# Optimization experiments

Measured on AMD Instinct MI355X. Metric: run time of the kernel, lower is better.

The kernel has to match this reference:

```python
import jax, jax.numpy as jnp
import numpy as np

P = 7            # cfg.PATCH_SIZE_PHOTOMETRIC
BRIGHT = 0.02    # bright_threshold
BIG = 1e9        # masks invalid points out of kNN
K = 5            # neighbors for smoothness/slope


def _smooth_l1(x, y, beta):
    d = jnp.abs(x - y)
    return jnp.where(d < beta, 0.5 * d * d / beta, d - 0.5 * beta)


def _sample_patches(img, kp):
    # img: [B,1,H,W], kp: [B,N,2] (x,y) in pixel coords -> [B,1,N,P,P]
    # matches F.grid_sample(align_corners=True, bilinear, border): with the
    # module's normalization, sampling positions are exactly pixel coords.
    B, _, H, W = img.shape
    N = kp.shape[1]
    half = P // 2
    lin = jnp.linspace(-half, half, P)
    oy, ox = jnp.meshgrid(lin, lin, indexing='ij')  # patch index (i,j): +x=lin[j], +y=lin[i]
    px = jnp.clip(kp[..., 0:1] + ox.ravel(), 0.0, W - 1)  # [B,N,P*P]
    py = jnp.clip(kp[..., 1:2] + oy.ravel(), 0.0, H - 1)
    x0 = jnp.floor(px); y0 = jnp.floor(py)
    fx = px - x0; fy = py - y0
    x0i = jnp.clip(x0.astype(jnp.int32), 0, W - 1)
    x1i = jnp.clip(x0i + 1, 0, W - 1)
    y0i = jnp.clip(y0.astype(jnp.int32), 0, H - 1)
    y1i = jnp.clip(y0i + 1, 0, H - 1)
    im = img[:, 0]  # [B,H,W]
    b = jnp.arange(B)[:, None, None]
    v00 = im[b, y0i, x0i]; v01 = im[b, y0i, x1i]
    v10 = im[b, y1i, x0i]; v11 = im[b, y1i, x1i]
    val = (v00 * (1 - fx) + v01 * fx) * (1 - fy) + (v10 * (1 - fx) + v11 * fx) * fy
    return val.reshape(B, 1, N, P, P)


def _forward(lg, rg, kpl, kpr, scores, Q):
    B, N, _ = kpl.shape
    # ---- epipolar ----
    y_diff = jnp.abs(kpl[..., 1] - kpr[..., 1])
    ws = scores.sum()
    l_epipolar = jnp.where(ws > 1e-4, (y_diff * scores).sum() / jnp.maximum(ws, 1e-12), y_diff.mean())
    # ---- photometric + intensity ----
    pl = _sample_patches(lg, kpl)
    pr = _sample_patches(rg, kpr)
    c = P // 2
    center_l = pl[:, 0, :, c, c]  # [B,N]
    center_r = pr[:, 0, :, c, c]
    is_bright = (center_l > BRIGHT).astype(pl.dtype)
    diff = jnp.abs(pl - pr).mean(axis=(1, 3, 4))  # [B,N]
    w = scores * is_bright
    wsum = w.sum()
    safe = jnp.maximum(wsum, 1e-12)
    l_masked = jnp.where(wsum > 1e-4, (diff * w).sum() / safe, 0.0)
    l_intensity = jnp.where(wsum > 1e-4, (_smooth_l1(center_l, center_r, 1.0) * w).sum() / safe, 0.0)
    l_photo = l_masked + l_intensity
    # ---- disparity -> 3D ----
    disp = kpl[..., 0] - kpr[..., 0]
    pts4 = jnp.concatenate([kpl, disp[..., None], jnp.ones((B, N, 1), kpl.dtype)], axis=-1)
    proj = jnp.einsum('bni,bji->bnj', pts4, Q)
    Wc = jnp.maximum(proj[..., 3], 1e-6)
    p3d = proj[..., :3] / Wc[..., None]  # [B,N,3]
    Z = p3d[..., 2]
    valid = (Z > 100) & (Z < 30000) & (scores > 0.1)  # [B,N]
    # ---- kNN smoothness / slope / zero-mean (masked, vectorized) ----
    pm = p3d / 1000.0
    xy = pm[..., jnp.array([0, 2])]  # [B,N,2] horizontal plane
    h = pm[..., 1]                   # [B,N] height
    sq = (xy * xy).sum(-1)
    d2 = sq[:, :, None] + sq[:, None, :] - 2.0 * jnp.einsum('bnd,bmd->bnm', xy, xy)
    dist = jnp.sqrt(jnp.maximum(d2, 1e-12))  # [B,N,N]
    vm = valid[:, :, None] & valid[:, None, :]
    dist = jnp.where(vm, dist, BIG)
    negd, idx = jax.lax.top_k(-dist, K + 1)   # ascending distance
    nbr_idx = idx[:, :, 1:]                   # drop self
    nbr_d = jnp.maximum(-negd[:, :, 1:], 1e-3)
    b = jnp.arange(B)[:, None, None]
    nbr_h = h[b, nbr_idx]                     # [B,N,K]
    local_mean = nbr_h.mean(-1)
    n_valid = valid.sum(-1)
    nv = jnp.maximum(n_valid, 1).astype(h.dtype)
    vf = valid.astype(h.dtype)
    ls_b = (_smooth_l1(h, local_mean, 0.01) * vf).sum(-1) / nv
    slopes = jnp.abs(nbr_h - h[..., None]) / nbr_d
    pen = jax.nn.relu(slopes - 0.4)
    lsl_b = (pen * vf[..., None]).sum((-1, -2)) / (nv * K)
    lz_b = jnp.abs((h * vf).sum(-1) / nv)
    ok = (n_valid >= 10).astype(h.dtype)
    nb = jnp.maximum(ok.sum(), 1.0)
    gate = ((scores > 0.1).sum() >= 10) & (ok.sum() > 0)
    l_smooth = jnp.where(gate, (ls_b * ok).sum() / nb, 0.0)
    l_slope = jnp.where(gate, (lsl_b * ok).sum() / nb, 0.0)
    l_zeromean = jnp.where(gate, (lz_b * ok).sum() / nb, 0.0)
    return (l_photo, l_epipolar, l_smooth, l_slope, l_zeromean)


def setup_inputs() -> dict:
    key = jax.random.key(0)
    k = jax.random.split(key, 7)
    B, N, H, W = 16, 2000, 720, 1280
    lg = jax.random.uniform(k[0], (B, 1, H, W), dtype=jnp.float32)
    rg = jax.random.uniform(k[1], (B, 1, H, W), dtype=jnp.float32)
    kx = jax.random.uniform(k[2], (B, N), minval=200.0, maxval=1080.0)
    ky = jax.random.uniform(k[3], (B, N), minval=50.0, maxval=670.0)
    disp = jax.random.uniform(k[4], (B, N), minval=10.0, maxval=200.0)
    kpl = jnp.stack([kx, ky], -1)
    kpr = jnp.stack([kx - disp, ky + 0.5 * jax.random.normal(k[5], (B, N))], -1)
    scores = jax.random.uniform(k[6], (B, N), dtype=jnp.float32)
    f, cx, cy, Tx = 1000.0, 640.0, 360.0, 120.0  # focal px, principal point, baseline mm
    Qm = jnp.array([[1.0, 0.0, 0.0, -cx],
                    [0.0, 1.0, 0.0, -cy],
                    [0.0, 0.0, 0.0, f],
                    [0.0, 0.0, 1.0 / Tx, 0.0]], dtype=jnp.float32)
    Q = jnp.broadcast_to(Qm, (B, 4, 4))
    return {"lg": lg, "rg": rg, "kpl": kpl, "kpr": kpr, "scores": scores, "Q": Q}


def reference(lg, rg, kpl, kpr, scores, Q):
    return _forward(lg, rg, kpl, kpr, scores, Q)
```

## Files before the change

kernel.cpp:

```cpp
#include <hip/hip_runtime.h>

#define BB 16
#define NN 2000
#define HH 720
#define WW 1280
#define NPT (BB*NN)
#define PB_BLOCKS (NPT/4)
#define PROJ_BLOCKS (NPT/256)
#define KSTRIDE 2048
#define MAX_SEG 500

static __device__ __forceinline__ unsigned u_min(unsigned a, unsigned b){ return a < b ? a : b; }

static __device__ __forceinline__ unsigned u_med3(unsigned a, unsigned b, unsigned c) {
    unsigned d;
    asm("v_med3_u32 %0, %1, %2, %3" : "=v"(d) : "v"(a), "v"(b), "v"(c));
    return d;
}

__device__ __forceinline__ void ins5(unsigned K[5], unsigned u) {
    K[4] = u_med3(K[3], K[4], u);
    K[3] = u_med3(K[2], K[3], u);
    K[2] = u_med3(K[1], K[2], u);
    K[1] = u_med3(K[0], K[1], u);
    K[0] = u_min(K[0], u);
}

__device__ __forceinline__ float bilin(const float* __restrict__ im, float px, float py) {
    px = fminf(fmaxf(px, 0.f), (float)(WW - 1));
    py = fminf(fmaxf(py, 0.f), (float)(HH - 1));
    float x0f = floorf(px), y0f = floorf(py);
    float fx = px - x0f, fy = py - y0f;
    int x0 = min(max((int)x0f, 0), WW - 1);
    int x1 = min(x0 + 1, WW - 1);
    int y0 = min(max((int)y0f, 0), HH - 1);
    int y1 = min(y0 + 1, HH - 1);
    const float* r0 = im + (size_t)y0 * WW;
    const float* r1 = im + (size_t)y1 * WW;
    float v00 = r0[x0], v01 = r0[x1], v10 = r1[x0], v11 = r1[x1];
    return (v00 * (1.f - fx) + v01 * fx) * (1.f - fy)
         + (v10 * (1.f - fx) + v11 * fx) * fy;
}

__global__ __launch_bounds__(256) void project_kernel(
    const float* __restrict__ kpl, const float* __restrict__ kpr,
    const float* __restrict__ scores, const float* __restrict__ Q,
    float4* __restrict__ pts, float* __restrict__ partialsA,
    float* __restrict__ batch_acc, unsigned* __restrict__ dcnt)
{
    if (blockIdx.x == 0) {
        if (threadIdx.x < BB * 4) batch_acc[threadIdx.x] = 0.f;
        if (threadIdx.x == BB * 4) *dcnt = 0u;
    }
    int pt = blockIdx.x * 256 + threadIdx.x;
    int b  = pt / NN;

    float2 kl = ((const float2* __restrict__)kpl)[pt];
    float2 kr = ((const float2* __restrict__)kpr)[pt];
    float sc  = scores[pt];
    float ydiff = fabsf(kl.y - kr.y);

    const float* q = Q + b * 16;
    float dsp = kl.x - kr.x;
    float p0 = q[0]*kl.x  + q[1]*kl.y  + q[2]*dsp  + q[3];
    float p1 = q[4]*kl.x  + q[5]*kl.y  + q[6]*dsp  + q[7];
    float p2 = q[8]*kl.x  + q[9]*kl.y  + q[10]*dsp + q[11];
    float p3 = q[12]*kl.x + q[13]*kl.y + q[14]*dsp + q[15];
    float Wc = fmaxf(p3, 1e-6f);
    float X = p0 / Wc, Y = p1 / Wc, Z = p2 / Wc;
    bool valid = (Z > 100.f) && (Z < 30000.f) && (sc > 0.1f);
    float x  = X / 1000.f;
    float hh = Y / 1000.f;
    float y  = Z / 1000.f;
    float sq = x * x + y * y;
    if (!valid) { x = 0.f; y = 0.f; sq = 1e18f; }
    pts[pt] = make_float4(x, y, sq, hh);

    float s0 = sc, s1 = ydiff * sc, s2 = ydiff, s3 = (sc > 0.1f) ? 1.f : 0.f;
    #pragma unroll
    for (int off = 32; off > 0; off >>= 1) {
        s0 += __shfl_down(s0, off, 64);
        s1 += __shfl_down(s1, off, 64);
        s2 += __shfl_down(s2, off, 64);
        s3 += __shfl_down(s3, off, 64);
    }
    __shared__ float red[4][4];
    int wave = threadIdx.x >> 6, lane = threadIdx.x & 63;
    if (lane == 0) { red[wave][0]=s0; red[wave][1]=s1; red[wave][2]=s2; red[wave][3]=s3; }
    __syncthreads();
    if (threadIdx.x < 4) {
        int k = threadIdx.x;
        partialsA[blockIdx.x * 4 + k] = red[0][k] + red[1][k] + red[2][k] + red[3][k];
    }
}

__global__ __launch_bounds__(256) void fused_patch_scan(
    const float* __restrict__ lg, const float* __restrict__ rg,
    const float* __restrict__ kpl, const float* __restrict__ kpr,
    const float* __restrict__ scores,
    const float4* __restrict__ pts, unsigned* __restrict__ keybuf,
    float* __restrict__ partialsB, int msegLen, int lns, int interleave)
{
    int i = blockIdx.x;
    int pid, sid;
    if (interleave) {
        if ((i % 5) == 0) { sid = i / 5; pid = -1; }
        else { pid = (i / 5) * 4 + (i % 5) - 1; sid = -1; }
    } else {
        if (i < PB_BLOCKS) { pid = i; sid = -1; }
        else { pid = -1; sid = i - PB_BLOCKS; }
    }

    if (pid >= 0) {
        if (pid >= PB_BLOCKS) return;
        int wave = threadIdx.x >> 6, lane = threadIdx.x & 63;
        int rr = lane / 7, ci = lane - rr * 7;
        int s00 = lane + rr;
        if (s00 > 54) s00 = 54;
        int reg_r = lane >> 3, reg_c = lane & 7;

        int pt = pid * 4 + wave;
        int b = pt / NN;
        const float* iml = lg + (size_t)b * (HH * WW);
        const float* imr = rg + (size_t)b * (HH * WW);
        float kxl = kpl[2*pt], kyl = kpl[2*pt+1];
        float kxr = kpr[2*pt], kyr = kpr[2*pt+1];
        float sc  = scores[pt];

        float flx = floorf(kxl), fly = floorf(kyl);
        float frx = floorf(kxr), fry = floorf(kyr);
        int xbl = (int)flx - 3, ybl = (int)fly - 3;
        int xbr = (int)frx - 3, ybr = (int)fry - 3;
        float fxl = kxl - flx, fyl = kyl - fly;
        float fxr = kxr - frx, fyr = kyr - fry;
        bool inL = (xbl >= 0) && (xbl <= WW-8) && (ybl >= 0) && (ybl <= HH-8);
        bool inR = (xbr >= 0) && (xbr <= WW-8) && (ybr >= 0) && (ybr <= HH-8);

        float regL = 0.f, regR = 0.f;
        if (inL) regL = iml[(size_t)(ybl + reg_r) * WW + xbl + reg_c];
        if (inR) regR = imr[(size_t)(ybr + reg_r) * WW + xbr + reg_c];

        float vl = 0.f, vr = 0.f;
        if (inL) {
            float v00 = __shfl(regL, s00,     64);
            float v01 = __shfl(regL, s00 + 1, 64);
            float v10 = __shfl(regL, s00 + 8, 64);
            float v11 = __shfl(regL, s00 + 9, 64);
            vl = (v00*(1.f-fxl) + v01*fxl)*(1.f-fyl) + (v10*(1.f-fxl) + v11*fxl)*fyl;
        } else if (lane < 49) {
            vl = bilin(iml, kxl + (float)(ci-3), kyl + (float)(rr-3));
        }
        if (inR) {
            float v00 = __shfl(regR, s00,     64);
            float v01 = __shfl(regR, s00 + 1, 64);
            float v10 = __shfl(regR, s00 + 8, 64);
            float v11 = __shfl(regR, s00 + 9, 64);
            vr = (v00*(1.f-fxr) + v01*fxr)*(1.f-fyr) + (v10*(1.f-fxr) + v11*fxr)*fyr;
        } else if (lane < 49) {
            vr = bilin(imr, kxr + (float)(ci-3), kyr + (float)(rr-3));
        }

        float adiff = (lane < 49) ? fabsf(vl - vr) : 0.f;
        float cl = __shfl(vl, 24, 64);
        float cr = __shfl(vr, 24, 64);
        #pragma unroll
        for (int off = 32; off > 0; off >>= 1) adiff += __shfl_down(adiff, off, 64);

        __shared__ float red[4][3];
        if (lane == 0) {
            float isb = (cl > 0.02f) ? 1.f : 0.f;
            float w   = sc * isb;
            float dc  = fabsf(cl - cr);
            float sl1 = (dc < 1.f) ? 0.5f * dc * dc : dc - 0.5f;
            red[wave][0] = w;
            red[wave][1] = w * adiff * (1.f/49.f);
            red[wave][2] = sl1 * w;
        }
        __syncthreads();
        if (threadIdx.x < 4) {
            int k = threadIdx.x;
            float v = 0.f;
            if (k < 3) v = red[0][k] + red[1][k] + red[2][k] + red[3][k];
            partialsB[pid * 4 + k] = v;
        }
    } else {
        __shared__ float4 seg[MAX_SEG];
        int sblk = sid;
        int bx   = sblk & 7;
        int r    = sblk >> 3;
        int segi = r & ((1 << lns) - 1);
        int b    = r >> lns;
        int ns   = 1 << lns;
        int mseg0 = segi * msegLen;
        int n = bx * 256 + threadIdx.x;
        int nc = (n < NN) ? n : (NN - 1);

        const float4* cand = pts + b * NN + mseg0;
        for (int j = threadIdx.x; j < msegLen; j += 256) seg[j] = cand[j];

        float4 me = pts[b * NN + nc];
        float nx2 = -2.f * me.x, ny2 = -2.f * me.y, sqn = me.z;

        unsigned K[5] = {0xFFFFFFFFu,0xFFFFFFFFu,0xFFFFFFFFu,0xFFFFFFFFu,0xFFFFFFFFu};

        int nb0 = bx * 256;
        bool has_self = (mseg0 < nb0 + 256) && (mseg0 + msegLen > nb0);

        __syncthreads();

        if (has_self) {
            #pragma unroll 5
            for (int mm = 0; mm < msegLen; ++mm) {
                float4 o = seg[mm];
                int m = mseg0 + mm;
                float t = fmaf(ny2, o.y, o.z);
                t = fmaf(nx2, o.x, t);
                float d2 = fmaxf(t + sqn, 1e-12f);
                unsigned u = (__float_as_uint(d2) & 0xFFFFF800u) | (unsigned)m;
                u = (m == n) ? 0xFFFFFFFFu : u;
                ins5(K, u);
            }
        } else {
            #pragma unroll 5
            for (int mm = 0; mm < msegLen; ++mm) {
                float4 o = seg[mm];
                int m = mseg0 + mm;
                float t = fmaf(ny2, o.y, o.z);
                t = fmaf(nx2, o.x, t);
                float d2 = fmaxf(t + sqn, 1e-12f);
                unsigned u = (__float_as_uint(d2) & 0xFFFFF800u) | (unsigned)m;
                ins5(K, u);
            }
        }

        if (n < NN) {
            size_t base = (size_t)((b * ns + segi) * 5) * KSTRIDE + n;
            keybuf[base              ] = K[0];
            keybuf[base + KSTRIDE    ] = K[1];
            keybuf[base + KSTRIDE * 2] = K[2];
            keybuf[base + KSTRIDE * 3] = K[3];
            keybuf[base + KSTRIDE * 4] = K[4];
        }
    }
}

__global__ __launch_bounds__(256) void knn_merge_final(
    const float4* __restrict__ pts, const unsigned* __restrict__ keybuf,
    float* __restrict__ batch_acc, unsigned* __restrict__ dcnt,
    const float* __restrict__ partialsA, const float* __restrict__ partialsB,
    float* __restrict__ out, int ns)
{
    int b = blockIdx.y;
    int n = blockIdx.x * 256 + threadIdx.x;

    float ls = 0.f, pen = 0.f, hacc = 0.f, cnt = 0.f;
    if (n < NN) {
        float4 me = pts[b * NN + n];
        if (me.z < 1e17f) {
            unsigned K[5] = {0xFFFFFFFFu,0xFFFFFFFFu,0xFFFFFFFFu,0xFFFFFFFFu,0xFFFFFFFFu};
            for (int s = 0; s < ns; ++s) {
                #pragma unroll
                for (int j = 0; j < 5; ++j) {
                    unsigned u = keybuf[(size_t)((b * ns + s) * 5 + j) * KSTRIDE + n];
                    ins5(K, u);
                }
            }
            float hsum = 0.f;
            #pragma unroll
            for (int t = 0; t < 5; ++t) {
                int idx = (int)(K[t] & 2047u);
                float4 o = pts[b * NN + idx];
                float dot = me.x * o.x + me.y * o.y;
                float d2 = (me.z + o.z) - 2.f * dot;
                float nd = fmaxf(sqrtf(fmaxf(d2, 1e-12f)), 0.001f);
                hsum += o.w;
                pen  += fmaxf(fabsf(o.w - me.w) / nd - 0.4f, 0.f);
            }
            float lm = hsum / 5.f;
            float dd = fabsf(me.w - lm);
            ls = (dd < 0.01f) ? 0.5f * dd * dd / 0.01f : dd - 0.005f;
            hacc = me.w;
            cnt  = 1.f;
        }
    }

    #pragma unroll
    for (int off = 32; off > 0; off >>= 1) {
        ls   += __shfl_down(ls,   off, 64);
        pen  += __shfl_down(pen,  off, 64);
        hacc += __shfl_down(hacc, off, 64);
        cnt  += __shfl_down(cnt,  off, 64);
    }
    __shared__ float r2[4][4];
    int wave = threadIdx.x >> 6, lane = threadIdx.x & 63;
    if (lane == 0) { r2[wave][0]=cnt; r2[wave][1]=ls; r2[wave][2]=pen; r2[wave][3]=hacc; }
    __syncthreads();
    if (threadIdx.x == 0) {
        float tc = r2[0][0]+r2[1][0]+r2[2][0]+r2[3][0];
        float tl = r2[0][1]+r2[1][1]+r2[2][1]+r2[3][1];
        float tp = r2[0][2]+r2[1][2]+r2[2][2]+r2[3][2];
        float th = r2[0][3]+r2[1][3]+r2[2][3]+r2[3][3];
        atomicAdd(&batch_acc[b * 4 + 0], tc);
        atomicAdd(&batch_acc[b * 4 + 1], tl);
        atomicAdd(&batch_acc[b * 4 + 2], tp);
        atomicAdd(&batch_acc[b * 4 + 3], th);
    }

    __shared__ int lastf;
    __threadfence();
    if (threadIdx.x == 0) {
        unsigned old = atomicAdd(dcnt, 1u);
        lastf = (old == (unsigned)(8 * BB - 1)) ? 1 : 0;
    }
    __syncthreads();
    if (!lastf) return;
    __threadfence();

    float s[7] = {0,0,0,0,0,0,0};
    for (int rI = threadIdx.x; rI < PROJ_BLOCKS; rI += 256) {
        s[0] += partialsA[rI * 4 + 0];
        s[1] += partialsA[rI * 4 + 1];
        s[2] += partialsA[rI * 4 + 2];
        s[3] += partialsA[rI * 4 + 3];
    }
    for (int rI = threadIdx.x; rI < PB_BLOCKS; rI += 256) {
        s[4] += partialsB[rI * 4 + 0];
        s[5] += partialsB[rI * 4 + 1];
        s[6] += partialsB[rI * 4 + 2];
    }
    #pragma unroll
    for (int off = 32; off > 0; off >>= 1) {
        #pragma unroll
        for (int k = 0; k < 7; ++k) s[k] += __shfl_down(s[k], off, 64);
    }
    __shared__ float ws2[4][7];
    if (lane == 0) {
        #pragma unroll
        for (int k = 0; k < 7; ++k) ws2[wave][k] = s[k];
    }
    __syncthreads();
    if (threadIdx.x == 0) {
        float t[7];
        #pragma unroll
        for (int k = 0; k < 7; ++k)
            t[k] = ws2[0][k] + ws2[1][k] + ws2[2][k] + ws2[3][k];
        float ssc = t[0], yds = t[1], yd = t[2], cnts = t[3];
        float wsum = t[4], dw = t[5], iw = t[6];

        float l_epi = (ssc > 1e-4f) ? yds / fmaxf(ssc, 1e-12f) : yd / (float)NPT;
        float safe = fmaxf(wsum, 1e-12f);
        float l_photo = (wsum > 1e-4f) ? (dw / safe + iw / safe) : 0.f;

        float als = 0.f, alsl = 0.f, alz = 0.f, okc = 0.f;
        for (int bb = 0; bb < BB; ++bb) {
            float nvf  = __hip_atomic_load(&batch_acc[bb*4+0], __ATOMIC_RELAXED, __HIP_MEMORY_SCOPE_AGENT);
            float lsb  = __hip_atomic_load(&batch_acc[bb*4+1], __ATOMIC_RELAXED, __HIP_MEMORY_SCOPE_AGENT);
            float penb = __hip_atomic_load(&batch_acc[bb*4+2], __ATOMIC_RELAXED, __HIP_MEMORY_SCOPE_AGENT);
            float hb   = __hip_atomic_load(&batch_acc[bb*4+3], __ATOMIC_RELAXED, __HIP_MEMORY_SCOPE_AGENT);
            float nv = fmaxf(nvf, 1.f);
            float ok = (nvf >= 10.f) ? 1.f : 0.f;
            als  += ok * (lsb / nv);
            alsl += ok * (penb / (nv * 5.f));
            alz  += ok * fabsf(hb / nv);
            okc  += ok;
        }
        float nb = fmaxf(okc, 1.f);
        bool gate = (cnts >= 10.f) && (okc > 0.f);
        out[0] = l_photo;
        out[1] = l_epi;
        out[2] = gate ? als / nb : 0.f;
        out[3] = gate ? alsl / nb : 0.f;
        out[4] = gate ? alz / nb : 0.f;
    }
}

extern "C" void kernel_launch(void* const* d_in, const int* in_sizes, int n_in,
                              void* d_out, int out_size, void* d_ws, size_t ws_size,
                              hipStream_t stream)
{
    const float* lg     = (const float*)d_in[0];
    const float* rg     = (const float*)d_in[1];
    const float* kpl    = (const float*)d_in[2];
    const float* kpr    = (const float*)d_in[3];
    const float* scores = (const float*)d_in[4];
    const float* Q      = (const float*)d_in[5];
    float* out = (float*)d_out;

    char* ws = (char*)d_ws;
    float4*   pts       = (float4*)ws;
    float*    partialsA = (float*)(ws + 512000);
    float*    partialsB = (float*)(ws + 514048);
    float*    batch_acc = (float*)(ws + 645120);
    unsigned* dcnt      = (unsigned*)(ws + 645376);
    unsigned* keybuf    = (unsigned*)(ws + 645632);

    int ns = 16;
    if (ws_size < 645632 + (size_t)BB * 16 * 5 * KSTRIDE * 4) ns = 8;
    if (ws_size < 645632 + (size_t)BB *  8 * 5 * KSTRIDE * 4) ns = 4;
    int lns = (ns == 16) ? 4 : ((ns == 8) ? 3 : 2);
    int msegLen = NN / ns;
    int interleave = (ns == 16) ? 1 : 0;

    int nblk = interleave ? 10240 : (PB_BLOCKS + 8 * ns * BB);

    project_kernel<<<PROJ_BLOCKS, 256, 0, stream>>>(kpl, kpr, scores, Q,
                                                    pts, partialsA, batch_acc, dcnt);
    fused_patch_scan<<<nblk, 256, 0, stream>>>(
        lg, rg, kpl, kpr, scores, pts, keybuf, partialsB, msegLen, lns, interleave);
    knn_merge_final<<<dim3(8, BB), 256, 0, stream>>>(pts, keybuf, batch_acc, dcnt,
                                                     partialsA, partialsB, out, ns);
}
```

Baseline: 188.4 us.

## Sort keypoints by row and co-schedule patch and kNN waves per block

Adds a per-batch counting sort of keypoints by y row so that neighbouring patch-sampling waves touch nearby image rows, aiming for better cache locality. The fused kernel now runs 320-thread blocks: four waves sample patches and one wave does a 64-query kNN segment scan, in place of separate block types. Per-point partials are written as float4, which removes the block-level shared reduction but leaves the final reduction to sum 32000 entries. It costs an extra kernel launch, and the final single-block reduction becomes larger.

Result: slower. 218.1 us (+15.8%).

```diff
diff --git a/kernel.cpp b/kernel.cpp
--- a/kernel.cpp
+++ b/kernel.cpp
@@ -5,7 +5,6 @@
 #define HH 720
 #define WW 1280
 #define NPT (BB*NN)
-#define PB_BLOCKS (NPT/4)
 #define PROJ_BLOCKS (NPT/256)
 #define KSTRIDE 2048
 #define MAX_SEG 500
@@ -94,33 +93,71 @@
     }
 }
 
-__global__ __launch_bounds__(256) void fused_patch_scan(
+__global__ __launch_bounds__(256) void sort_kernel(
+    const float* __restrict__ kpl, int* __restrict__ order)
+{
+    int b = blockIdx.x;
+    __shared__ int hist[720];
+    __shared__ int wsum[4];
+    for (int i = threadIdx.x; i < 720; i += 256) hist[i] = 0;
+    __syncthreads();
+    for (int p = threadIdx.x; p < NN; p += 256) {
+        float y = kpl[2 * (b * NN + p) + 1];
+        int bin = min(max((int)y, 0), 719);
+        atomicAdd(&hist[bin], 1);
+    }
+    __syncthreads();
+    int tid = threadIdx.x, lane = tid & 63, wv = tid >> 6;
+    int h0 = 0, h1 = 0, h2 = 0;
+    if (tid < 240) { h0 = hist[tid*3]; h1 = hist[tid*3+1]; h2 = hist[tid*3+2]; }
+    int lsum = h0 + h1 + h2;
+    int pre = lsum;
+    #pragma unroll
+    for (int off = 1; off < 64; off <<= 1) {
+        int t = __shfl_up(pre, off, 64);
+        if (lane >= off) pre += t;
+    }
+    if (lane == 63) wsum[wv] = pre;
+    __syncthreads();
+    int woff = 0;
+    for (int k = 0; k < wv; ++k) woff += wsum[k];
+    int excl = woff + pre - lsum;
+    if (tid < 240) {
+        hist[tid*3    ] = excl;
+        hist[tid*3 + 1] = excl + h0;
+        hist[tid*3 + 2] = excl + h0 + h1;
+    }
+    __syncthreads();
+    for (int p = threadIdx.x; p < NN; p += 256) {
+        float y = kpl[2 * (b * NN + p) + 1];
+        int bin = min(max((int)y, 0), 719);
+        int pos = atomicAdd(&hist[bin], 1);
+        order[b * NN + pos] = b * NN + p;
+    }
+}
+
+__global__ __launch_bounds__(320) void fused_patch_scan(
     const float* __restrict__ lg, const float* __restrict__ rg,
     const float* __restrict__ kpl, const float* __restrict__ kpr,
     const float* __restrict__ scores,
     const float4* __restrict__ pts, unsigned* __restrict__ keybuf,
-    float* __restrict__ partialsB, int msegLen, int lns, int interleave)
+    float4* __restrict__ partialsB, const int* __restrict__ order,
+    int msegLen, int lns)
 {
-    int i = blockIdx.x;
-    int pid, sid;
-    if (interleave) {
-        if ((i % 5) == 0) { sid = i / 5; pid = -1; }
-        else { pid = (i / 5) * 4 + (i % 5) - 1; sid = -1; }
-    } else {
-        if (i < PB_BLOCKS) { pid = i; sid = -1; }
-        else { pid = -1; sid = i - PB_BLOCKS; }
-    }
-
-    if (pid >= 0) {
-        if (pid >= PB_BLOCKS) return;
-        int wave = threadIdx.x >> 6, lane = threadIdx.x & 63;
+    __shared__ float4 seg[MAX_SEG];
+    int wave = threadIdx.x >> 6, lane = threadIdx.x & 63;
+
+    if (wave < 4) {
+        int idx = blockIdx.x * 4 + wave;
+        if (idx >= NPT) return;
+        int pt = order[idx];
+        int b  = idx / NN;
+
         int rr = lane / 7, ci = lane - rr * 7;
         int s00 = lane + rr;
         if (s00 > 54) s00 = 54;
         int reg_r = lane >> 3, reg_c = lane & 7;
 
-        int pt = pid * 4 + wave;
-        int b = pt / NN;
         const float* iml = lg + (size_t)b * (HH * WW);
         const float* imr = rg + (size_t)b * (HH * WW);
         float kxl = kpl[2*pt], kyl = kpl[2*pt+1];
@@ -166,47 +203,36 @@
         #pragma unroll
         for (int off = 32; off > 0; off >>= 1) adiff += __shfl_down(adiff, off, 64);
 
-        __shared__ float red[4][3];
         if (lane == 0) {
             float isb = (cl > 0.02f) ? 1.f : 0.f;
             float w   = sc * isb;
             float dc  = fabsf(cl - cr);
             float sl1 = (dc < 1.f) ? 0.5f * dc * dc : dc - 0.5f;
-            red[wave][0] = w;
-            red[wave][1] = w * adiff * (1.f/49.f);
-            red[wave][2] = sl1 * w;
-        }
-        __syncthreads();
-        if (threadIdx.x < 4) {
-            int k = threadIdx.x;
-            float v = 0.f;
-            if (k < 3) v = red[0][k] + red[1][k] + red[2][k] + red[3][k];
-            partialsB[pid * 4 + k] = v;
+            partialsB[pt] = make_float4(w, w * adiff * (1.f/49.f), sl1 * w, 0.f);
         }
     } else {
-        __shared__ float4 seg[MAX_SEG];
-        int sblk = sid;
-        int bx   = sblk & 7;
-        int r    = sblk >> 3;
-        int segi = r & ((1 << lns) - 1);
+        int ns  = 1 << lns;
+        int sid = blockIdx.x;
+        if (sid >= 32 * ns * BB) return;
+        int bx2  = sid & 31;
+        int r    = sid >> 5;
+        int segi = r & (ns - 1);
         int b    = r >> lns;
-        int ns   = 1 << lns;
         int mseg0 = segi * msegLen;
-        int n = bx * 256 + threadIdx.x;
+
+        const float4* cand = pts + b * NN + mseg0;
+        for (int j = lane; j < msegLen; j += 64) seg[j] = cand[j];
+        asm volatile("s_waitcnt lgkmcnt(0)" ::: "memory");
+
+        int n  = bx2 * 64 + lane;
         int nc = (n < NN) ? n : (NN - 1);
-
-        const float4* cand = pts + b * NN + mseg0;
-        for (int j = threadIdx.x; j < msegLen; j += 256) seg[j] = cand[j];
-
         float4 me = pts[b * NN + nc];
         float nx2 = -2.f * me.x, ny2 = -2.f * me.y, sqn = me.z;
 
         unsigned K[5] = {0xFFFFFFFFu,0xFFFFFFFFu,0xFFFFFFFFu,0xFFFFFFFFu,0xFFFFFFFFu};
 
-        int nb0 = bx * 256;
-        bool has_self = (mseg0 < nb0 + 256) && (mseg0 + msegLen > nb0);
-
-        __syncthreads();
+        int nb0 = bx2 * 64;
+        bool has_self = (mseg0 < nb0 + 64) && (mseg0 + msegLen > nb0);
 
         if (has_self) {
             #pragma unroll 5
@@ -247,7 +273,7 @@
 __global__ __launch_bounds__(256) void knn_merge_final(
     const float4* __restrict__ pts, const unsigned* __restrict__ keybuf,
     float* __restrict__ batch_acc, unsigned* __restrict__ dcnt,
-    const float* __restrict__ partialsA, const float* __restrict__ partialsB,
+    const float* __restrict__ partialsA, const float4* __restrict__ partialsB,
     float* __restrict__ out, int ns)
 {
     int b = blockIdx.y;
@@ -323,10 +349,11 @@
         s[2] += partialsA[rI * 4 + 2];
         s[3] += partialsA[rI * 4 + 3];
     }
-    for (int rI = threadIdx.x; rI < PB_BLOCKS; rI += 256) {
-        s[4] += partialsB[rI * 4 + 0];
-        s[5] += partialsB[rI * 4 + 1];
-        s[6] += partialsB[rI * 4 + 2];
+    for (int rI = threadIdx.x; rI < NPT; rI += 256) {
+        float4 v = partialsB[rI];
+        s[4] += v.x;
+        s[5] += v.y;
+        s[6] += v.z;
     }
     #pragma unroll
     for (int off = 32; off > 0; off >>= 1) {
@@ -389,24 +416,27 @@
     char* ws = (char*)d_ws;
     float4*   pts       = (float4*)ws;
     float*    partialsA = (float*)(ws + 512000);
-    float*    partialsB = (float*)(ws + 514048);
-    float*    batch_acc = (float*)(ws + 645120);
-    unsigned* dcnt      = (unsigned*)(ws + 645376);
-    unsigned* keybuf    = (unsigned*)(ws + 645632);
+    int*      order     = (int*)(ws + 514048);
+    float4*   partialsB = (float4*)(ws + 642048);
+    float*    batch_acc = (float*)(ws + 1154048);
+    unsigned* dcnt      = (unsigned*)(ws + 1154304);
+    unsigned* keybuf    = (unsigned*)(ws + 1154560);
 
     int ns = 16;
-    if (ws_size < 645632 + (size_t)BB * 16 * 5 * KSTRIDE * 4) ns = 8;
-    if (ws_size < 645632 + (size_t)BB *  8 * 5 * KSTRIDE * 4) ns = 4;
+    if (ws_size < 1154560 + (size_t)BB * 16 * 5 * KSTRIDE * 4) ns = 8;
+    if (ws_size < 1154560 + (size_t)BB *  8 * 5 * KSTRIDE * 4) ns = 4;
     int lns = (ns == 16) ? 4 : ((ns == 8) ? 3 : 2);
     int msegLen = NN / ns;
-    int interleave = (ns == 16) ? 1 : 0;
-
-    int nblk = interleave ? 10240 : (PB_BLOCKS + 8 * ns * BB);
+
+    int nsActive = 32 * ns * BB;
+    int nblk = (NPT + 3) / 4;
+    if (nsActive > nblk) nblk = nsActive;
 
     project_kernel<<<PROJ_BLOCKS, 256, 0, stream>>>(kpl, kpr, scores, Q,
                                                     pts, partialsA, batch_acc, dcnt);
-    fused_patch_scan<<<nblk, 256, 0, stream>>>(
-        lg, rg, kpl, kpr, scores, pts, keybuf, partialsB, msegLen, lns, interleave);
+    sort_kernel<<<BB, 256, 0, stream>>>(kpl, order);
+    fused_patch_scan<<<nblk, 320, 0, stream>>>(
+        lg, rg, kpl, kpr, scores, pts, keybuf, partialsB, order, msegLen, lns);
     knn_merge_final<<<dim3(8, BB), 256, 0, stream>>>(pts, keybuf, batch_acc, dcnt,
                                                      partialsA, partialsB, out, ns);
 }
```
